# Optimization experiments

Hardware: AMD Instinct MI355X
Metric: run time of the kernel (lower is better)

Reference implementation:

```python
import jax, jax.numpy as jnp
import numpy as np

B, S, HID = 2, 2048, 3072
H, HKV, D = 16, 8, 256
ROPE_THETA = 10000.0
NEG_INF = -1e9


def setup_inputs() -> dict:
    key = jax.random.key(0)
    ks = jax.random.split(key, 5)
    hidden_states = jax.random.normal(ks[0], (B, S, HID), jnp.float32)
    # rotary frequencies: complex freqs_cis = cos + i*sin, shape (B, S, D//2)
    inv_freq = 1.0 / (ROPE_THETA ** (np.arange(0, D, 2, dtype=np.float32) / D))
    ang = np.arange(S, dtype=np.float32)[:, None] * inv_freq[None, :]  # (S, D//2)
    cos = jnp.asarray(np.broadcast_to(np.cos(ang)[None], (B, S, D // 2)).copy())
    sin = jnp.asarray(np.broadcast_to(np.sin(ang)[None], (B, S, D // 2)).copy())
    causal = jnp.tril(jnp.ones((S, S), dtype=bool))
    mask = jnp.where(causal, 0.0, NEG_INF).astype(jnp.float32)[None, None]  # (1,1,S,S)
    wq = jax.random.normal(ks[1], (HID, H * D), jnp.float32) * 0.02
    wk = jax.random.normal(ks[2], (HID, HKV * D), jnp.float32) * 0.02
    wv = jax.random.normal(ks[3], (HID, HKV * D), jnp.float32) * 0.02
    wo = jax.random.normal(ks[4], (H * D, HID), jnp.float32) * 0.02
    return {"hidden_states": hidden_states, "cos": cos, "sin": sin, "mask": mask,
            "wq": wq, "wk": wk, "wv": wv, "wo": wo}


def _apply_rotary(x, cos, sin):
    # x: (B, S, Hx, D). Torch code forms complex pairs (x[..., :D/2], x[..., D/2:])
    # and multiplies by freqs_cis = cos + i*sin, then re-concats real||imag halves.
    half = x.shape[-1] // 2
    x1, x2 = x[..., :half], x[..., half:]
    c = cos[:, :, None, :]  # (B, S, 1, D/2)
    s = sin[:, :, None, :]
    return jnp.concatenate([x1 * c - x2 * s, x1 * s + x2 * c], axis=-1)


def reference(hidden_states, cos, sin, mask, wq, wk, wv, wo):
    b, s, _ = hidden_states.shape
    q = (hidden_states @ wq).reshape(b, s, H, D)
    k = (hidden_states @ wk).reshape(b, s, HKV, D)
    v = (hidden_states @ wv).reshape(b, s, HKV, D)
    q = _apply_rotary(q, cos, sin)
    k = _apply_rotary(k, cos, sin)
    # GQA: group query heads per kv head instead of materializing repeated K/V
    g = H // HKV
    qg = q.reshape(b, s, HKV, g, D)
    scaling = D ** (-0.5)
    scores = jnp.einsum('bskgd,btkd->bkgst', qg, k) * scaling  # (B,HKV,G,S,S)
    scores = scores + mask[:, :, None]  # broadcast (1,1,1,S,S)
    probs = jax.nn.softmax(scores, axis=-1)
    out = jnp.einsum('bkgst,btkd->bskgd', probs, v).reshape(b, s, H * D)
    return out @ wo
```

## Files before the change

kernel.cpp:

```cpp
#include <hip/hip_runtime.h>

typedef short bf16x8 __attribute__((ext_vector_type(8)));
typedef float f32x4 __attribute__((ext_vector_type(4)));

#define S_LEN 2048
#define NHQ 16
#define NKV 8
#define HD 256

__device__ __forceinline__ unsigned short f2bf(float f){
  unsigned u = __float_as_uint(f);
  unsigned r = (u + 0x7FFFu + ((u >> 16) & 1u)) >> 16;
  return (unsigned short)r;
}
__device__ __forceinline__ float bf2f(unsigned short h){
  return __uint_as_float(((unsigned)h) << 16);
}
__device__ __forceinline__ unsigned pack2(float a, float b){
  return (unsigned)f2bf(a) | ((unsigned)f2bf(b) << 16);
}

__global__ void k_conv(const float* __restrict__ in, unsigned short* __restrict__ out, int n){
  int i = (blockIdx.x * 256 + threadIdx.x) * 4;
  if (i < n){
    float4 v = *(const float4*)&in[i];
    ushort4 o;
    o.x = f2bf(v.x); o.y = f2bf(v.y); o.z = f2bf(v.z); o.w = f2bf(v.w);
    *(ushort4*)&out[i] = o;
  }
}

__global__ void k_tconv(const float* __restrict__ in, unsigned short* __restrict__ out, int R, int C){
  __shared__ float tile[32][33];
  int c0 = blockIdx.x * 32, r0 = blockIdx.y * 32;
  int tx = threadIdx.x, ty = threadIdx.y;
  for (int i = 0; i < 4; i++)
    tile[ty + i*8][tx] = in[(size_t)(r0 + ty + i*8) * C + c0 + tx];
  __syncthreads();
  for (int i = 0; i < 4; i++)
    out[(size_t)(c0 + ty + i*8) * R + r0 + tx] = f2bf(tile[tx][ty + i*8]);
}

__global__ void k_vtrans(const unsigned short* __restrict__ V, unsigned short* __restrict__ VT){
  __shared__ unsigned short tile[32][40];
  int s0 = blockIdx.x * 32, d0 = blockIdx.y * 32, bz = blockIdx.z;
  int b = bz >> 3, kv = bz & 7;
  int tx = threadIdx.x, ty = threadIdx.y;
  for (int i = 0; i < 4; i++)
    tile[ty + i*8][tx] = V[(size_t)(b * S_LEN + s0 + ty + i*8) * (NKV*HD) + kv*HD + d0 + tx];
  __syncthreads();
  for (int i = 0; i < 4; i++)
    VT[((size_t)(bz * HD + d0 + ty + i*8)) * S_LEN + s0 + tx] = tile[tx][ty + i*8];
}

__global__ void k_rope(unsigned short* buf, const float* __restrict__ cosb,
                       const float* __restrict__ sinb, int lgnh){
  int idx = blockIdx.x * 256 + threadIdx.x;
  int d = idx & 127;
  int h = (idx >> 7) & ((1 << lgnh) - 1);
  int t = idx >> (7 + lgnh);
  float c = cosb[t * 128 + d], s = sinb[t * 128 + d];
  size_t base = ((size_t)t << (lgnh + 8)) + ((size_t)h << 8) + d;
  float x1 = bf2f(buf[base]), x2 = bf2f(buf[base + 128]);
  buf[base]       = f2bf(x1 * c - x2 * s);
  buf[base + 128] = f2bf(x1 * s + x2 * c);
}

__global__ __launch_bounds__(256) void k_gemm_bt(const unsigned short* __restrict__ A,
    const unsigned short* __restrict__ Bt, void* __restrict__ Cp,
    int M, int N, int K, int out_bf16){
  __shared__ __align__(16) unsigned short smem[2 * 128 * 64];
  unsigned short* As = smem;
  unsigned short* Bs = smem + 128 * 64;
  int tid = threadIdx.x;
  int lane = tid & 63, wave = tid >> 6, quad = lane >> 4, l16 = lane & 15;
  int wm = wave >> 1, wn = wave & 1;
  int bm0 = blockIdx.y * 128, bn0 = blockIdx.x * 128;
  f32x4 acc[4][4] = {};
  for (int k0 = 0; k0 < K; k0 += 64){
    __syncthreads();
    for (int it = 0; it < 4; it++){
      int slot = it * 256 + tid;
      int row = slot >> 3, c = slot & 7;
      int pc = c ^ (row & 7);
      *(uint4*)&As[row * 64 + pc * 8] = *(const uint4*)&A[(size_t)(bm0 + row) * K + k0 + c * 8];
      *(uint4*)&Bs[row * 64 + pc * 8] = *(const uint4*)&Bt[(size_t)(bn0 + row) * K + k0 + c * 8];
    }
    __syncthreads();
    for (int ks = 0; ks < 2; ks++){
      bf16x8 af[4], bfr[4];
      for (int mt = 0; mt < 4; mt++){
        int row = wm * 64 + mt * 16 + l16;
        int pc = (ks * 4 + quad) ^ (row & 7);
        af[mt] = *(const bf16x8*)&As[row * 64 + pc * 8];
      }
      for (int nt = 0; nt < 4; nt++){
        int row = wn * 64 + nt * 16 + l16;
        int pc = (ks * 4 + quad) ^ (row & 7);
        bfr[nt] = *(const bf16x8*)&Bs[row * 64 + pc * 8];
      }
      for (int mt = 0; mt < 4; mt++)
        for (int nt = 0; nt < 4; nt++)
          acc[mt][nt] = __builtin_amdgcn_mfma_f32_16x16x32_bf16(af[mt], bfr[nt], acc[mt][nt], 0, 0, 0);
    }
  }
  float* Ct = (float*)smem;
  for (int p = 0; p < 2; p++){
    __syncthreads();
    if (wm == p){
      for (int mt = 0; mt < 4; mt++)
        for (int nt = 0; nt < 4; nt++)
          for (int r = 0; r < 4; r++)
            Ct[(mt * 16 + quad * 4 + r) * 128 + wn * 64 + nt * 16 + l16] = acc[mt][nt][r];
    }
    __syncthreads();
    if (out_bf16){
      unsigned short* O = (unsigned short*)Cp;
      for (int j = 0; j < 4; j++){
        int chunk = j * 256 + tid;
        int row = chunk >> 4, col = (chunk & 15) * 8;
        const float* src = &Ct[row * 128 + col];
        uint4 o;
        o.x = pack2(src[0], src[1]);
        o.y = pack2(src[2], src[3]);
        o.z = pack2(src[4], src[5]);
        o.w = pack2(src[6], src[7]);
        *(uint4*)&O[(size_t)(bm0 + p * 64 + row) * N + bn0 + col] = o;
      }
    } else {
      float* O = (float*)Cp;
      for (int j = 0; j < 8; j++){
        int chunk = j * 256 + tid;
        int row = chunk >> 5, col = (chunk & 31) * 4;
        *(float4*)&O[(size_t)(bm0 + p * 64 + row) * N + bn0 + col] = *(const float4*)&Ct[row * 128 + col];
      }
    }
  }
}

__global__ __launch_bounds__(256) void k_flash(const unsigned short* __restrict__ Q,
    const unsigned short* __restrict__ Kg, const unsigned short* __restrict__ VTg,
    unsigned short* __restrict__ Og){
  __shared__ __align__(16) unsigned short smem[32 * 264 + 256 * 40 + 4 * 16 * 40];
  unsigned short* Ks  = smem;
  unsigned short* VTs = smem + 32 * 264;
  unsigned short* Ps  = VTs + 256 * 40;
  int tid = threadIdx.x;
  int lane = tid & 63, wave = tid >> 6, quad = lane >> 4, l16 = lane & 15;
  int qt = blockIdx.x, hd_ = blockIdx.y;
  int b = hd_ >> 4, h = hd_ & 15, kv = h >> 1;

  bf16x8 qf[8];
  {
    size_t qoff = ((size_t)(b * S_LEN + qt * 64 + wave * 16 + l16)) * (NHQ * HD) + (size_t)h * HD;
    for (int ks = 0; ks < 8; ks++)
      qf[ks] = *(const bf16x8*)&Q[qoff + ks * 32 + quad * 8];
  }
  f32x4 acc[16] = {};
  float mrow[4], lrow[4];
  for (int r = 0; r < 4; r++){ mrow[r] = -1e30f; lrow[r] = 0.f; }
  int qmin = qt * 64 + wave * 16;
  int nkt = qt * 2 + 2;
  const float L2E = 1.4426950408889634f;
  const float scale = 0.0625f;

  for (int kt = 0; kt < nkt; kt++){
    __syncthreads();
    for (int it = 0; it < 4; it++){
      int slot = it * 256 + tid;
      int kr = slot >> 5, c = slot & 31;
      *(uint4*)&Ks[kr * 264 + c * 8] =
          *(const uint4*)&Kg[(size_t)(b * S_LEN + kt * 32 + kr) * (NKV*HD) + (size_t)kv * HD + c * 8];
      int dd = slot >> 2, c2 = slot & 3;
      *(uint4*)&VTs[dd * 40 + c2 * 8] =
          *(const uint4*)&VTg[((size_t)((b * NKV + kv) * HD + dd)) * S_LEN + kt * 32 + c2 * 8];
    }
    __syncthreads();
    if (kt * 32 > qmin + 15) continue;

    f32x4 sv[2] = {};
    for (int ks = 0; ks < 8; ks++){
      for (int nt = 0; nt < 2; nt++){
        bf16x8 kf = *(const bf16x8*)&Ks[(nt * 16 + l16) * 264 + ks * 32 + quad * 8];
        sv[nt] = __builtin_amdgcn_mfma_f32_16x16x32_bf16(qf[ks], kf, sv[nt], 0, 0, 0);
      }
    }
    float pv[2][4], tmax[4];
    for (int r = 0; r < 4; r++){
      int qr = qmin + quad * 4 + r;
      float mx = -1e30f;
      for (int nt = 0; nt < 2; nt++){
        int key = kt * 32 + nt * 16 + l16;
        float v = sv[nt][r] * scale;
        if (key > qr) v = -1e30f;
        pv[nt][r] = v;
        mx = fmaxf(mx, v);
      }
      tmax[r] = mx;
    }
    for (int off = 1; off < 16; off <<= 1)
      for (int r = 0; r < 4; r++)
        tmax[r] = fmaxf(tmax[r], __shfl_xor(tmax[r], off, 64));
    float alpha[4];
    for (int r = 0; r < 4; r++){
      float mn = fmaxf(mrow[r], tmax[r]);
      alpha[r] = exp2f((mrow[r] - mn) * L2E);
      mrow[r] = mn;
    }
    float pb[2][4], psum[4] = {0.f, 0.f, 0.f, 0.f};
    for (int nt = 0; nt < 2; nt++)
      for (int r = 0; r < 4; r++){
        float p = exp2f((pv[nt][r] - mrow[r]) * L2E);
        pb[nt][r] = p; psum[r] += p;
      }
    for (int off = 1; off < 16; off <<= 1)
      for (int r = 0; r < 4; r++)
        psum[r] += __shfl_xor(psum[r], off, 64);
    for (int r = 0; r < 4; r++) lrow[r] = lrow[r] * alpha[r] + psum[r];
    for (int i = 0; i < 16; i++)
      for (int r = 0; r < 4; r++) acc[i][r] *= alpha[r];
    int pbase = wave * 16 * 40;
    for (int nt = 0; nt < 2; nt++)
      for (int r = 0; r < 4; r++)
        Ps[pbase + (quad * 4 + r) * 40 + nt * 16 + l16] = f2bf(pb[nt][r]);
    bf16x8 pa = *(const bf16x8*)&Ps[pbase + l16 * 40 + quad * 8];
    for (int nt = 0; nt < 16; nt++){
      bf16x8 vf = *(const bf16x8*)&VTs[(nt * 16 + l16) * 40 + quad * 8];
      acc[nt] = __builtin_amdgcn_mfma_f32_16x16x32_bf16(pa, vf, acc[nt], 0, 0, 0);
    }
  }
  float inv[4];
  for (int r = 0; r < 4; r++) inv[r] = 1.0f / lrow[r];
  __syncthreads();
  unsigned short* Ot = smem + wave * 16 * 256;
  for (int nt = 0; nt < 16; nt++)
    for (int r = 0; r < 4; r++)
      Ot[(quad * 4 + r) * 256 + nt * 16 + l16] = f2bf(acc[nt][r] * inv[r]);
  size_t obase = ((size_t)(b * S_LEN + qt * 64 + wave * 16)) * (NHQ * HD) + (size_t)h * HD;
  for (int j = 0; j < 8; j++){
    int chunk = j * 64 + lane;
    int row = chunk >> 5, col = (chunk & 31) * 8;
    *(uint4*)&Og[obase + (size_t)row * (NHQ * HD) + col] = *(const uint4*)&Ot[row * 256 + col];
  }
}

extern "C" void kernel_launch(void* const* d_in, const int* in_sizes, int n_in,
                              void* d_out, int out_size, void* d_ws, size_t ws_size,
                              hipStream_t stream){
  const float* hid  = (const float*)d_in[0];
  const float* cosb = (const float*)d_in[1];
  const float* sinb = (const float*)d_in[2];
  const float* wq = (const float*)d_in[4];
  const float* wk = (const float*)d_in[5];
  const float* wv = (const float*)d_in[6];
  const float* wo = (const float*)d_in[7];

  char* ws = (char*)d_ws;
  size_t off = 0;
  auto alloc = [&](size_t bytes) -> void* {
    void* p = ws + off; off += (bytes + 255) & ~(size_t)255; return p;
  };
  unsigned short* Xbf = (unsigned short*)alloc(4096ull * 3072 * 2);
  unsigned short* WqT = (unsigned short*)alloc(4096ull * 3072 * 2);
  unsigned short* WkT = (unsigned short*)alloc(2048ull * 3072 * 2);
  unsigned short* WvT = (unsigned short*)alloc(2048ull * 3072 * 2);
  unsigned short* WoT = (unsigned short*)alloc(3072ull * 4096 * 2);
  unsigned short* Qb  = (unsigned short*)alloc(4096ull * 4096 * 2);
  unsigned short* Kb  = (unsigned short*)alloc(4096ull * 2048 * 2);
  unsigned short* Vb  = (unsigned short*)alloc(4096ull * 2048 * 2);
  unsigned short* VTb = (unsigned short*)alloc(4096ull * 2048 * 2);
  unsigned short* Ab  = (unsigned short*)alloc(4096ull * 4096 * 2);

  k_conv<<<12288, 256, 0, stream>>>(hid, Xbf, 4096 * 3072);
  k_tconv<<<dim3(128, 96), dim3(32, 8), 0, stream>>>(wq, WqT, 3072, 4096);
  k_tconv<<<dim3(64, 96),  dim3(32, 8), 0, stream>>>(wk, WkT, 3072, 2048);
  k_tconv<<<dim3(64, 96),  dim3(32, 8), 0, stream>>>(wv, WvT, 3072, 2048);
  k_tconv<<<dim3(96, 128), dim3(32, 8), 0, stream>>>(wo, WoT, 4096, 3072);
  k_gemm_bt<<<dim3(32, 32), 256, 0, stream>>>(Xbf, WqT, Qb, 4096, 4096, 3072, 1);
  k_gemm_bt<<<dim3(16, 32), 256, 0, stream>>>(Xbf, WkT, Kb, 4096, 2048, 3072, 1);
  k_gemm_bt<<<dim3(16, 32), 256, 0, stream>>>(Xbf, WvT, Vb, 4096, 2048, 3072, 1);
  k_rope<<<32768, 256, 0, stream>>>(Qb, cosb, sinb, 4);
  k_rope<<<16384, 256, 0, stream>>>(Kb, cosb, sinb, 3);
  k_vtrans<<<dim3(64, 8, 16), dim3(32, 8), 0, stream>>>(Vb, VTb);
  k_flash<<<dim3(32, 32), 256, 0, stream>>>(Qb, Kb, VTb, Ab);
  k_gemm_bt<<<dim3(24, 32), 256, 0, stream>>>(Ab, WoT, d_out, 4096, 3072, 4096, 0);
}
```

Before: 1.050 ms.

## Share KV tiles across GQA head pair, double-buffer loads, balance causal tiles

The flash kernel now runs 512-thread blocks per (batch, kv head), so both query heads in a GQA group share each K/V tile staged in LDS, halving K/V global traffic. Each block handles query tile p and then 31-p, which balances the causal triangle work across blocks. K/V loads for the next tile are issued into registers before computing the current tile, and LDS is double-buffered so only one barrier is needed per iteration. In exchange the grid shrinks to 256 blocks, each with higher register and LDS use, which may reduce occupancy and latency hiding.

New measurement: 902.7 us. 14.0% less time.

```diff
diff --git a/kernel.cpp b/kernel.cpp
--- a/kernel.cpp
+++ b/kernel.cpp
@@ -138,109 +138,134 @@
   }
 }
 
-__global__ __launch_bounds__(256) void k_flash(const unsigned short* __restrict__ Q,
+__global__ __launch_bounds__(512, 2) void k_flash(const unsigned short* __restrict__ Q,
     const unsigned short* __restrict__ Kg, const unsigned short* __restrict__ VTg,
     unsigned short* __restrict__ Og){
-  __shared__ __align__(16) unsigned short smem[32 * 264 + 256 * 40 + 4 * 16 * 40];
-  unsigned short* Ks  = smem;
-  unsigned short* VTs = smem + 32 * 264;
-  unsigned short* Ps  = VTs + 256 * 40;
+  __shared__ __align__(16) unsigned short smem[2 * (32*264 + 256*40) + 8 * 16 * 40];
+  const int BUFSZ = 32*264 + 256*40;
   int tid = threadIdx.x;
   int lane = tid & 63, wave = tid >> 6, quad = lane >> 4, l16 = lane & 15;
-  int qt = blockIdx.x, hd_ = blockIdx.y;
-  int b = hd_ >> 4, h = hd_ & 15, kv = h >> 1;
-
-  bf16x8 qf[8];
-  {
-    size_t qoff = ((size_t)(b * S_LEN + qt * 64 + wave * 16 + l16)) * (NHQ * HD) + (size_t)h * HD;
-    for (int ks = 0; ks < 8; ks++)
-      qf[ks] = *(const bf16x8*)&Q[qoff + ks * 32 + quad * 8];
-  }
-  f32x4 acc[16] = {};
-  float mrow[4], lrow[4];
-  for (int r = 0; r < 4; r++){ mrow[r] = -1e30f; lrow[r] = 0.f; }
-  int qmin = qt * 64 + wave * 16;
-  int nkt = qt * 2 + 2;
+  int hig = wave & 1, rowgrp = wave >> 1;
+  int p = blockIdx.x, bkv = blockIdx.y;
+  int b = bkv >> 3, kv = bkv & 7;
+  int h = kv * 2 + hig;
   const float L2E = 1.4426950408889634f;
   const float scale = 0.0625f;
 
-  for (int kt = 0; kt < nkt; kt++){
-    __syncthreads();
-    for (int it = 0; it < 4; it++){
-      int slot = it * 256 + tid;
+  size_t kgbase = (size_t)(b * S_LEN) * (NKV*HD) + (size_t)kv * HD;
+  size_t vtbase = ((size_t)(b * NKV + kv) * HD) * S_LEN;
+  unsigned short* Ps = smem + 2 * BUFSZ + wave * (16 * 40);
+
+  for (int ph = 0; ph < 2; ph++){
+    int qt = ph ? (31 - p) : p;
+    int qmin = qt * 64 + rowgrp * 16;
+    int nkt = qt * 2 + 2;
+
+    bf16x8 qf[8];
+    {
+      size_t qoff = ((size_t)(b * S_LEN + qt * 64 + rowgrp * 16 + l16)) * (NHQ * HD) + (size_t)h * HD;
+      for (int ks = 0; ks < 8; ks++)
+        qf[ks] = *(const bf16x8*)&Q[qoff + ks * 32 + quad * 8];
+    }
+    f32x4 acc[16] = {};
+    float mrow[4], lrow[4];
+    for (int r = 0; r < 4; r++){ mrow[r] = -1e30f; lrow[r] = 0.f; }
+
+    uint4 stk[2], stv[2];
+    for (int it = 0; it < 2; it++){
+      int slot = it * 512 + tid;
       int kr = slot >> 5, c = slot & 31;
-      *(uint4*)&Ks[kr * 264 + c * 8] =
-          *(const uint4*)&Kg[(size_t)(b * S_LEN + kt * 32 + kr) * (NKV*HD) + (size_t)kv * HD + c * 8];
+      stk[it] = *(const uint4*)&Kg[kgbase + (size_t)(kr) * (NKV*HD) + c * 8];
       int dd = slot >> 2, c2 = slot & 3;
-      *(uint4*)&VTs[dd * 40 + c2 * 8] =
-          *(const uint4*)&VTg[((size_t)((b * NKV + kv) * HD + dd)) * S_LEN + kt * 32 + c2 * 8];
-    }
-    __syncthreads();
-    if (kt * 32 > qmin + 15) continue;
-
-    f32x4 sv[2] = {};
-    for (int ks = 0; ks < 8; ks++){
-      for (int nt = 0; nt < 2; nt++){
-        bf16x8 kf = *(const bf16x8*)&Ks[(nt * 16 + l16) * 264 + ks * 32 + quad * 8];
-        sv[nt] = __builtin_amdgcn_mfma_f32_16x16x32_bf16(qf[ks], kf, sv[nt], 0, 0, 0);
-      }
-    }
-    float pv[2][4], tmax[4];
-    for (int r = 0; r < 4; r++){
-      int qr = qmin + quad * 4 + r;
-      float mx = -1e30f;
-      for (int nt = 0; nt < 2; nt++){
-        int key = kt * 32 + nt * 16 + l16;
-        float v = sv[nt][r] * scale;
-        if (key > qr) v = -1e30f;
-        pv[nt][r] = v;
-        mx = fmaxf(mx, v);
-      }
-      tmax[r] = mx;
-    }
-    for (int off = 1; off < 16; off <<= 1)
+      stv[it] = *(const uint4*)&VTg[vtbase + (size_t)dd * S_LEN + c2 * 8];
+    }
+
+    for (int kt = 0; kt < nkt; kt++){
+      unsigned short* Ks  = smem + (kt & 1) * BUFSZ;
+      unsigned short* VTs = Ks + 32 * 264;
+      for (int it = 0; it < 2; it++){
+        int slot = it * 512 + tid;
+        int kr = slot >> 5, c = slot & 31;
+        *(uint4*)&Ks[kr * 264 + c * 8] = stk[it];
+        int dd = slot >> 2, c2 = slot & 3;
+        *(uint4*)&VTs[dd * 40 + c2 * 8] = stv[it];
+      }
+      if (kt + 1 < nkt){
+        for (int it = 0; it < 2; it++){
+          int slot = it * 512 + tid;
+          int kr = slot >> 5, c = slot & 31;
+          stk[it] = *(const uint4*)&Kg[kgbase + (size_t)((kt + 1) * 32 + kr) * (NKV*HD) + c * 8];
+          int dd = slot >> 2, c2 = slot & 3;
+          stv[it] = *(const uint4*)&VTg[vtbase + (size_t)dd * S_LEN + (kt + 1) * 32 + c2 * 8];
+        }
+      }
+      __syncthreads();
+      if (kt * 32 > qmin + 15) continue;
+
+      f32x4 sv[2] = {};
+      for (int ks = 0; ks < 8; ks++){
+        for (int nt = 0; nt < 2; nt++){
+          bf16x8 kf = *(const bf16x8*)&Ks[(nt * 16 + l16) * 264 + ks * 32 + quad * 8];
+          sv[nt] = __builtin_amdgcn_mfma_f32_16x16x32_bf16(qf[ks], kf, sv[nt], 0, 0, 0);
+        }
+      }
+      float pv[2][4], tmax[4];
+      for (int r = 0; r < 4; r++){
+        int qr = qmin + quad * 4 + r;
+        float mx = -1e30f;
+        for (int nt = 0; nt < 2; nt++){
+          int key = kt * 32 + nt * 16 + l16;
+          float v = sv[nt][r] * scale;
+          if (key > qr) v = -1e30f;
+          pv[nt][r] = v;
+          mx = fmaxf(mx, v);
+        }
+        tmax[r] = mx;
+      }
+      for (int off = 1; off < 16; off <<= 1)
+        for (int r = 0; r < 4; r++)
+          tmax[r] = fmaxf(tmax[r], __shfl_xor(tmax[r], off, 64));
+      float alpha[4];
+      for (int r = 0; r < 4; r++){
+        float mn = fmaxf(mrow[r], tmax[r]);
+        alpha[r] = exp2f((mrow[r] - mn) * L2E);
+        mrow[r] = mn;
+      }
+      float pb[2][4], psum[4] = {0.f, 0.f, 0.f, 0.f};
+      for (int nt = 0; nt < 2; nt++)
+        for (int r = 0; r < 4; r++){
+          float pe = exp2f((pv[nt][r] - mrow[r]) * L2E);
+          pb[nt][r] = pe; psum[r] += pe;
+        }
+      for (int off = 1; off < 16; off <<= 1)
+        for (int r = 0; r < 4; r++)
+          psum[r] += __shfl_xor(psum[r], off, 64);
+      for (int r = 0; r < 4; r++) lrow[r] = lrow[r] * alpha[r] + psum[r];
+      for (int i = 0; i < 16; i++)
+        for (int r = 0; r < 4; r++) acc[i][r] *= alpha[r];
+      for (int nt = 0; nt < 2; nt++)
+        for (int r = 0; r < 4; r++)
+          Ps[(quad * 4 + r) * 40 + nt * 16 + l16] = f2bf(pb[nt][r]);
+      bf16x8 pa = *(const bf16x8*)&Ps[l16 * 40 + quad * 8];
+      for (int nt = 0; nt < 16; nt++){
+        bf16x8 vf = *(const bf16x8*)&VTs[(nt * 16 + l16) * 40 + quad * 8];
+        acc[nt] = __builtin_amdgcn_mfma_f32_16x16x32_bf16(pa, vf, acc[nt], 0, 0, 0);
+      }
+    }
+    float inv[4];
+    for (int r = 0; r < 4; r++) inv[r] = 1.0f / lrow[r];
+    __syncthreads();
+    unsigned short* Ot = smem + wave * (16 * 256);
+    for (int nt = 0; nt < 16; nt++)
       for (int r = 0; r < 4; r++)
-        tmax[r] = fmaxf(tmax[r], __shfl_xor(tmax[r], off, 64));
-    float alpha[4];
-    for (int r = 0; r < 4; r++){
-      float mn = fmaxf(mrow[r], tmax[r]);
-      alpha[r] = exp2f((mrow[r] - mn) * L2E);
-      mrow[r] = mn;
-    }
-    float pb[2][4], psum[4] = {0.f, 0.f, 0.f, 0.f};
-    for (int nt = 0; nt < 2; nt++)
-      for (int r = 0; r < 4; r++){
-        float p = exp2f((pv[nt][r] - mrow[r]) * L2E);
-        pb[nt][r] = p; psum[r] += p;
-      }
-    for (int off = 1; off < 16; off <<= 1)
-      for (int r = 0; r < 4; r++)
-        psum[r] += __shfl_xor(psum[r], off, 64);
-    for (int r = 0; r < 4; r++) lrow[r] = lrow[r] * alpha[r] + psum[r];
-    for (int i = 0; i < 16; i++)
-      for (int r = 0; r < 4; r++) acc[i][r] *= alpha[r];
-    int pbase = wave * 16 * 40;
-    for (int nt = 0; nt < 2; nt++)
-      for (int r = 0; r < 4; r++)
-        Ps[pbase + (quad * 4 + r) * 40 + nt * 16 + l16] = f2bf(pb[nt][r]);
-    bf16x8 pa = *(const bf16x8*)&Ps[pbase + l16 * 40 + quad * 8];
-    for (int nt = 0; nt < 16; nt++){
-      bf16x8 vf = *(const bf16x8*)&VTs[(nt * 16 + l16) * 40 + quad * 8];
-      acc[nt] = __builtin_amdgcn_mfma_f32_16x16x32_bf16(pa, vf, acc[nt], 0, 0, 0);
-    }
-  }
-  float inv[4];
-  for (int r = 0; r < 4; r++) inv[r] = 1.0f / lrow[r];
-  __syncthreads();
-  unsigned short* Ot = smem + wave * 16 * 256;
-  for (int nt = 0; nt < 16; nt++)
-    for (int r = 0; r < 4; r++)
-      Ot[(quad * 4 + r) * 256 + nt * 16 + l16] = f2bf(acc[nt][r] * inv[r]);
-  size_t obase = ((size_t)(b * S_LEN + qt * 64 + wave * 16)) * (NHQ * HD) + (size_t)h * HD;
-  for (int j = 0; j < 8; j++){
-    int chunk = j * 64 + lane;
-    int row = chunk >> 5, col = (chunk & 31) * 8;
-    *(uint4*)&Og[obase + (size_t)row * (NHQ * HD) + col] = *(const uint4*)&Ot[row * 256 + col];
+        Ot[(quad * 4 + r) * 256 + nt * 16 + l16] = f2bf(acc[nt][r] * inv[r]);
+    size_t obase = ((size_t)(b * S_LEN + qt * 64 + rowgrp * 16)) * (NHQ * HD) + (size_t)h * HD;
+    for (int j = 0; j < 8; j++){
+      int chunk = j * 64 + lane;
+      int row = chunk >> 5, col = (chunk & 31) * 8;
+      *(uint4*)&Og[obase + (size_t)row * (NHQ * HD) + col] = *(const uint4*)&Ot[row * 256 + col];
+    }
+    __syncthreads();
   }
 }
 
@@ -282,6 +307,6 @@
   k_rope<<<32768, 256, 0, stream>>>(Qb, cosb, sinb, 4);
   k_rope<<<16384, 256, 0, stream>>>(Kb, cosb, sinb, 3);
   k_vtrans<<<dim3(64, 8, 16), dim3(32, 8), 0, stream>>>(Vb, VTb);
-  k_flash<<<dim3(32, 32), 256, 0, stream>>>(Qb, Kb, VTb, Ab);
+  k_flash<<<dim3(16, 16), 512, 0, stream>>>(Qb, Kb, VTb, Ab);
   k_gemm_bt<<<dim3(24, 32), 256, 0, stream>>>(Ab, WoT, d_out, 4096, 3072, 4096, 0);
 }
```
